# Optimization experiments

Measured on AMD Instinct MI355X. Metric: run time of the kernel, lower is better.

## Reference

```python
import jax, jax.numpy as jnp
import numpy as np


def fwht(x):
    """Normalized fast Walsh-Hadamard transform over the last dim (power of 2).
    Equivalent to x @ H_n / sqrt(n) with H symmetric, so it serves as both
    matmul_hadU and matmul_hadUt in QuIP#."""
    n = x.shape[-1]
    steps = int(np.log2(n))
    assert 1 << steps == n
    shape = x.shape
    x = x.reshape(-1, n)
    h = 1
    for _ in range(steps):
        x = x.reshape(-1, n // (2 * h), 2, h)
        a = x[:, :, 0, :]
        b = x[:, :, 1, :]
        x = jnp.stack([a + b, a - b], axis=2).reshape(-1, n)
        h *= 2
    return (x * np.float32(1.0 / np.sqrt(n))).reshape(shape)


def setup_inputs() -> dict:
    key = jax.random.key(0)
    ks = jax.random.split(key, 9)
    B, S = 4, 2048
    n_in, n_out, codesz, cb_size, rank = 4096, 4096, 4, 256, 64
    inputs = {
        "input": jax.random.normal(ks[0], (B, S, n_in), dtype=jnp.float32),
        "Qidxs": jax.random.randint(ks[1], (n_out, n_in // codesz), 0, cb_size, dtype=jnp.int32),
        "D4_CB": jax.random.normal(ks[2], (cb_size, codesz), dtype=jnp.float32),
        # SU / SV are random sign (+-1) vectors from the randomized Hadamard transform
        "SU": jnp.where(jax.random.bernoulli(ks[3], 0.5, (n_in,)), 1.0, -1.0).astype(jnp.float32),
        "SV": jnp.where(jax.random.bernoulli(ks[4], 0.5, (n_out,)), 1.0, -1.0).astype(jnp.float32),
        "Wscale": jnp.float32(0.9),
        "A": jax.random.normal(ks[5], (n_out, rank), dtype=jnp.float32) * 0.02,
        "B": jax.random.normal(ks[6], (rank, n_in), dtype=jnp.float32) * 0.02,
        # positive per-input-channel rescale
        "scaleWH": jax.random.uniform(ks[7], (n_in,), dtype=jnp.float32, minval=0.5, maxval=1.5),
    }
    return inputs


def reference(input, Qidxs, D4_CB, SU, SV, Wscale, A, B, scaleWH):
    n_out, n_groups = Qidxs.shape
    codesz = D4_CB.shape[1]
    n_in = n_groups * codesz
    lead = input.shape[:-1]

    x = input.reshape(-1, n_in)            # [T, n_in]
    x = x / scaleWH                        # rescale_WH
    x = x * SU                             # input sign flips
    x = fwht(x)                            # matmul_hadUt
    Bx = x @ B.T                           # [T, rank] low-rank path

    # Dequantize: gather codebook vectors and flatten groups -> [n_out, n_in]
    W_hat = D4_CB[Qidxs].reshape(n_out, n_in)
    z = x @ W_hat.T                        # [T, n_out]

    z = z * Wscale
    z = z + Bx @ A.T                       # low-rank correction
    z = fwht(z)                            # matmul_hadU on output dim
    z = z * SV                             # output sign flips
    return z.reshape(*lead, n_out)
```

## Files before the change

kernel.cpp:

```cpp
#include <hip/hip_runtime.h>
#include <hip/hip_bf16.h>
#include <stdint.h>

typedef __attribute__((ext_vector_type(8))) short short8;
typedef __attribute__((ext_vector_type(4))) float floatx4;

#define GLOAD_LDS16(gptr, lptr)                                                     \
  __builtin_amdgcn_global_load_lds(                                                 \
      (const __attribute__((address_space(1))) void*)(gptr),                        \
      (__attribute__((address_space(3))) void*)(lptr), 16, 0, 0)

__device__ inline void fwht16(float v[16]) {
#pragma unroll
    for (int s = 0; s < 4; ++s) {
        const int h = 1 << s;
#pragma unroll
        for (int k = 0; k < 16; k += 2 * h)
#pragma unroll
            for (int j = 0; j < h; ++j) {
                float a = v[k + j], b = v[k + j + h];
                v[k + j] = a + b;
                v[k + j + h] = a - b;
            }
    }
}

__global__ __launch_bounds__(256) void decode_weff(
    const int* __restrict__ Qidxs, const float* __restrict__ D4_CB,
    const float* __restrict__ Wscale_p, const float* __restrict__ A,
    const float* __restrict__ B, __hip_bfloat16* __restrict__ W_eff)
{
    __shared__ __align__(16) float As[64 * 64];
    __shared__ __align__(16) float CB[256 * 4];
    const int t = threadIdx.x;
    const int oBase = blockIdx.y * 64;
    const int iBase = blockIdx.x * 256;

    const float4* A4 = (const float4*)(A + (long)oBase * 64);
    float4* As4 = (float4*)As;
#pragma unroll
    for (int u = 0; u < 4; ++u) As4[t + u * 256] = A4[t + u * 256];
    ((float4*)CB)[t] = ((const float4*)D4_CB)[t];
    __syncthreads();

    const float wscale = Wscale_p[0];
    const int i = iBase + t;
    float bcol[64];
#pragma unroll
    for (int r = 0; r < 64; ++r) bcol[r] = B[r * 4096 + i];

    const int g = i >> 2;
    const int sub = i & 3;

    for (int oo = 0; oo < 64; ++oo) {
        const int o = oBase + oo;
        const float4* arow = (const float4*)&As[oo * 64];
        float acc = 0.f;
#pragma unroll
        for (int r4 = 0; r4 < 16; ++r4) {
            float4 a4 = arow[r4];
            acc += a4.x * bcol[4 * r4 + 0] + a4.y * bcol[4 * r4 + 1] +
                   a4.z * bcol[4 * r4 + 2] + a4.w * bcol[4 * r4 + 3];
        }
        const int q = Qidxs[(long)o * 1024 + g];
        const float w = wscale * CB[q * 4 + sub] + acc;
        W_eff[(long)o * 4096 + i] = __float2bfloat16(w);
    }
}

__global__ __launch_bounds__(256) void fwht_in_kernel(
    const float* __restrict__ x, const float* __restrict__ SU,
    const float* __restrict__ sWH, __hip_bfloat16* __restrict__ xh)
{
    __shared__ float row[4096 + 256];
    const int t = threadIdx.x;
    const long base = (long)blockIdx.x * 4096;
    float v[16];

#pragma unroll
    for (int u = 0; u < 16; ++u) {
        int e = u * 256 + t;
        v[u] = x[base + e] / sWH[e] * SU[e];
    }
    fwht16(v);
#pragma unroll
    for (int u = 0; u < 16; ++u) {
        int e = u * 256 + t;
        row[e + (e >> 4)] = v[u];
    }
    __syncthreads();

    const int lo = t & 15, hi = t >> 4;
#pragma unroll
    for (int u = 0; u < 16; ++u) v[u] = row[hi * 272 + u * 17 + lo];
    fwht16(v);
#pragma unroll
    for (int u = 0; u < 16; ++u) row[hi * 272 + u * 17 + lo] = v[u];
    __syncthreads();

#pragma unroll
    for (int u = 0; u < 16; ++u) v[u] = row[t * 17 + u];
    fwht16(v);

    short8 o0, o1;
#pragma unroll
    for (int u = 0; u < 8; ++u) {
        __hip_bfloat16 b = __float2bfloat16(v[u] * 0.015625f);
        o0[u] = *(short*)&b;
    }
#pragma unroll
    for (int u = 0; u < 8; ++u) {
        __hip_bfloat16 b = __float2bfloat16(v[8 + u] * 0.015625f);
        o1[u] = *(short*)&b;
    }
    *(short8*)(xh + base + t * 16) = o0;
    *(short8*)(xh + base + t * 16 + 8) = o1;
}

__global__ __launch_bounds__(256) void gemm_bt(
    const __hip_bfloat16* __restrict__ xh,
    const __hip_bfloat16* __restrict__ wf,
    __hip_bfloat16* __restrict__ z)
{
    __shared__ __align__(16) __hip_bfloat16 lA[128 * 32];
    __shared__ __align__(16) __hip_bfloat16 lB[128 * 32];
    const int t = threadIdx.x;
    const int lane = t & 63;
    const int wv = t >> 6;
    const int wm = (wv >> 1) * 64;
    const int wn = (wv & 1) * 64;
    const long mBase = (long)blockIdx.y * 128;
    const long nBase = (long)blockIdx.x * 128;

    const int srow = wv * 32 + (lane >> 2);
    const int skoff = (((lane & 3) ^ ((lane >> 3) & 3)) * 8);
    const __hip_bfloat16* gA = xh + (mBase + srow) * 4096 + skoff;
    const __hip_bfloat16* gB = wf + (nBase + srow) * 4096 + skoff;
    const long rstep = 16L * 4096;
    __hip_bfloat16* lA0 = &lA[(wv * 32) * 32];
    __hip_bfloat16* lA1 = &lA[(wv * 32 + 16) * 32];
    __hip_bfloat16* lB0 = &lB[(wv * 32) * 32];
    __hip_bfloat16* lB1 = &lB[(wv * 32 + 16) * 32];

    floatx4 acc[4][4] = {};
    const int fr = lane & 15;
    const int q = lane >> 4;
    const int fq = (q ^ ((fr >> 1) & 3)) * 8;

    for (int kt = 0; kt < 4096; kt += 32) {
        GLOAD_LDS16(gA + kt, lA0);
        GLOAD_LDS16(gA + kt + rstep, lA1);
        GLOAD_LDS16(gB + kt, lB0);
        GLOAD_LDS16(gB + kt + rstep, lB1);
        __syncthreads();

        short8 af[4], bfr[4];
#pragma unroll
        for (int i = 0; i < 4; ++i)
            af[i] = *(const short8*)&lA[(wm + i * 16 + fr) * 32 + fq];
#pragma unroll
        for (int j = 0; j < 4; ++j)
            bfr[j] = *(const short8*)&lB[(wn + j * 16 + fr) * 32 + fq];
#pragma unroll
        for (int i = 0; i < 4; ++i)
#pragma unroll
            for (int j = 0; j < 4; ++j)
                acc[i][j] = __builtin_amdgcn_mfma_f32_16x16x32_bf16(
                    af[i], bfr[j], acc[i][j], 0, 0, 0);
        __syncthreads();
    }

    const int q4 = (lane >> 4) * 4;
#pragma unroll
    for (int i = 0; i < 4; ++i)
#pragma unroll
        for (int j = 0; j < 4; ++j)
#pragma unroll
            for (int r = 0; r < 4; ++r) {
                const long rrow = mBase + wm + i * 16 + q4 + r;
                const long ccol = nBase + wn + j * 16 + fr;
                z[rrow * 4096 + ccol] = __float2bfloat16(acc[i][j][r]);
            }
}

__global__ __launch_bounds__(256) void fwht_out_kernel(
    const __hip_bfloat16* __restrict__ z, const float* __restrict__ SV,
    float* __restrict__ out)
{
    __shared__ float row[4096 + 256];
    const int t = threadIdx.x;
    const long base = (long)blockIdx.x * 4096;
    float v[16];

#pragma unroll
    for (int u = 0; u < 16; ++u) {
        int e = u * 256 + t;
        v[u] = __bfloat162float(z[base + e]);
    }
    fwht16(v);
#pragma unroll
    for (int u = 0; u < 16; ++u) {
        int e = u * 256 + t;
        row[e + (e >> 4)] = v[u];
    }
    __syncthreads();

    const int lo = t & 15, hi = t >> 4;
#pragma unroll
    for (int u = 0; u < 16; ++u) v[u] = row[hi * 272 + u * 17 + lo];
    fwht16(v);
#pragma unroll
    for (int u = 0; u < 16; ++u) row[hi * 272 + u * 17 + lo] = v[u];
    __syncthreads();

#pragma unroll
    for (int u = 0; u < 16; ++u) v[u] = row[t * 17 + u];
    fwht16(v);

    const float4* svv = (const float4*)(SV + t * 16);
    float4* ov = (float4*)(out + base + t * 16);
#pragma unroll
    for (int c = 0; c < 4; ++c) {
        float4 s = svv[c];
        float4 f;
        f.x = v[4 * c + 0] * s.x * 0.015625f;
        f.y = v[4 * c + 1] * s.y * 0.015625f;
        f.z = v[4 * c + 2] * s.z * 0.015625f;
        f.w = v[4 * c + 3] * s.w * 0.015625f;
        ov[c] = f;
    }
}

extern "C" void kernel_launch(void* const* d_in, const int* in_sizes, int n_in,
                              void* d_out, int out_size, void* d_ws, size_t ws_size,
                              hipStream_t stream)
{
    const float* input  = (const float*)d_in[0];
    const int*   Qidxs  = (const int*)d_in[1];
    const float* D4_CB  = (const float*)d_in[2];
    const float* SU     = (const float*)d_in[3];
    const float* SV     = (const float*)d_in[4];
    const float* Wscale = (const float*)d_in[5];
    const float* A      = (const float*)d_in[6];
    const float* B      = (const float*)d_in[7];
    const float* sWH    = (const float*)d_in[8];
    float* out = (float*)d_out;

    char* ws = (char*)d_ws;
    __hip_bfloat16* weff = (__hip_bfloat16*)ws;
    __hip_bfloat16* xh   = (__hip_bfloat16*)(ws + (32L << 20));
    __hip_bfloat16* zbuf = (__hip_bfloat16*)(ws + (32L << 20) + (64L << 20));

    decode_weff<<<dim3(16, 64), 256, 0, stream>>>(Qidxs, D4_CB, Wscale, A, B, weff);
    fwht_in_kernel<<<8192, 256, 0, stream>>>(input, SU, sWH, xh);
    gemm_bt<<<dim3(32, 64), 256, 0, stream>>>(xh, weff, zbuf);
    fwht_out_kernel<<<8192, 256, 0, stream>>>(zbuf, SV, out);
}
```

Measured before the change: 663.1 us.

## Rewrite GEMM as 256x256 double-buffered pipelined tile with 8 waves

Replaces the 128x128, BK=32 single-buffered bf16 GEMM with a 256x256, BK=64 tile run by 512 threads. LDS is double-buffered, and global-to-LDS loads for the next k-step are interleaved with four MFMA quarter-phases using explicit barriers, waitcnt and setprio. The goal is to hide load latency and raise data reuse per LDS byte. It uses 128KB of LDS and many accumulator registers, which limits occupancy, and the hand-managed waitcnt and barriers carry correctness risk.

```diff
diff --git a/kernel.cpp b/kernel.cpp
--- a/kernel.cpp
+++ b/kernel.cpp
@@ -9,6 +9,11 @@
   __builtin_amdgcn_global_load_lds(                                                 \
       (const __attribute__((address_space(1))) void*)(gptr),                        \
       (__attribute__((address_space(3))) void*)(lptr), 16, 0, 0)
+
+#define FENCE() asm volatile("" ::: "memory")
+#define BARRIER() do { FENCE(); __builtin_amdgcn_s_barrier(); FENCE(); } while (0)
+#define WAIT_LGKM0() do { asm volatile("s_waitcnt lgkmcnt(0)" ::: "memory"); \
+                          __builtin_amdgcn_sched_barrier(0); } while (0)
 
 __device__ inline void fwht16(float v[16]) {
 #pragma unroll
@@ -117,69 +122,137 @@
     *(short8*)(xh + base + t * 16 + 8) = o1;
 }
 
-__global__ __launch_bounds__(256) void gemm_bt(
+__global__ __launch_bounds__(512, 2) void gemm_bt(
     const __hip_bfloat16* __restrict__ xh,
     const __hip_bfloat16* __restrict__ wf,
     __hip_bfloat16* __restrict__ z)
 {
-    __shared__ __align__(16) __hip_bfloat16 lA[128 * 32];
-    __shared__ __align__(16) __hip_bfloat16 lB[128 * 32];
+    __shared__ __align__(16) __hip_bfloat16 sA[2][256 * 64];
+    __shared__ __align__(16) __hip_bfloat16 sB[2][256 * 64];
+
     const int t = threadIdx.x;
     const int lane = t & 63;
     const int wv = t >> 6;
-    const int wm = (wv >> 1) * 64;
-    const int wn = (wv & 1) * 64;
-    const long mBase = (long)blockIdx.y * 128;
-    const long nBase = (long)blockIdx.x * 128;
-
-    const int srow = wv * 32 + (lane >> 2);
-    const int skoff = (((lane & 3) ^ ((lane >> 3) & 3)) * 8);
-    const __hip_bfloat16* gA = xh + (mBase + srow) * 4096 + skoff;
-    const __hip_bfloat16* gB = wf + (nBase + srow) * 4096 + skoff;
-    const long rstep = 16L * 4096;
-    __hip_bfloat16* lA0 = &lA[(wv * 32) * 32];
-    __hip_bfloat16* lA1 = &lA[(wv * 32 + 16) * 32];
-    __hip_bfloat16* lB0 = &lB[(wv * 32) * 32];
-    __hip_bfloat16* lB1 = &lB[(wv * 32 + 16) * 32];
-
-    floatx4 acc[4][4] = {};
+    const int wm = wv >> 2;
+    const int wn = wv & 3;
+    const long mBase = (long)blockIdx.y * 256;
+    const long nBase = (long)blockIdx.x * 256;
+
+    const int grow = t >> 3;
+    const int gcol = ((t & 7) ^ (grow & 7)) * 8;
+    const __hip_bfloat16* gA = xh + (mBase + grow) * 4096 + gcol;
+    const __hip_bfloat16* gB = wf + (nBase + grow) * 4096 + gcol;
+    const int lrow = wv * 8;
+
     const int fr = lane & 15;
-    const int q = lane >> 4;
-    const int fq = (q ^ ((fr >> 1) & 3)) * 8;
-
-    for (int kt = 0; kt < 4096; kt += 32) {
-        GLOAD_LDS16(gA + kt, lA0);
-        GLOAD_LDS16(gA + kt + rstep, lA1);
-        GLOAD_LDS16(gB + kt, lB0);
-        GLOAD_LDS16(gB + kt + rstep, lB1);
-        __syncthreads();
-
-        short8 af[4], bfr[4];
-#pragma unroll
-        for (int i = 0; i < 4; ++i)
-            af[i] = *(const short8*)&lA[(wm + i * 16 + fr) * 32 + fq];
-#pragma unroll
-        for (int j = 0; j < 4; ++j)
-            bfr[j] = *(const short8*)&lB[(wn + j * 16 + fr) * 32 + fq];
-#pragma unroll
-        for (int i = 0; i < 4; ++i)
-#pragma unroll
-            for (int j = 0; j < 4; ++j)
-                acc[i][j] = __builtin_amdgcn_mfma_f32_16x16x32_bf16(
-                    af[i], bfr[j], acc[i][j], 0, 0, 0);
-        __syncthreads();
-    }
-
-    const int q4 = (lane >> 4) * 4;
-#pragma unroll
-    for (int i = 0; i < 4; ++i)
-#pragma unroll
-        for (int j = 0; j < 4; ++j)
+    const int c2 = lane >> 4;
+    const int slot0 = ((c2 ^ (fr & 7)) * 8);
+
+    floatx4 acc[8][4] = {};
+    short8 afr[4][2];
+    short8 bfr[4][2];
+
+    auto stage = [&](int buf, int isA, int halfRow, int kt) {
+        const __hip_bfloat16* g =
+            (isA ? gA : gB) + (long)halfRow * 4096 + (long)kt * 64;
+        __hip_bfloat16* l =
+            (isA ? &sA[buf][0] : &sB[buf][0]) + (halfRow + lrow) * 64;
+        GLOAD_LDS16(g, l);
+        GLOAD_LDS16(g + 64L * 4096, l + 64 * 64);
+    };
+    auto ldA = [&](int buf, int mhalf) {
+        const __hip_bfloat16* base =
+            &sA[buf][0] + (wm * 128 + mhalf * 64 + fr) * 64;
+#pragma unroll
+        for (int m = 0; m < 4; ++m) {
+            afr[m][0] = *(const short8*)(base + m * 16 * 64 + slot0);
+            afr[m][1] = *(const short8*)(base + m * 16 * 64 + (slot0 ^ 32));
+        }
+    };
+    auto ldB2 = [&](int buf, int npair) {
+        const __hip_bfloat16* base =
+            &sB[buf][0] + (wn * 64 + npair * 32 + fr) * 64;
+#pragma unroll
+        for (int n = 0; n < 2; ++n) {
+            bfr[npair * 2 + n][0] = *(const short8*)(base + n * 16 * 64 + slot0);
+            bfr[npair * 2 + n][1] = *(const short8*)(base + n * 16 * 64 + (slot0 ^ 32));
+        }
+    };
+    auto mma16 = [&](int mh, int np) {
+#pragma unroll
+        for (int m = 0; m < 4; ++m)
+#pragma unroll
+            for (int n = 0; n < 2; ++n)
+#pragma unroll
+                for (int kh = 0; kh < 2; ++kh)
+                    acc[mh * 4 + m][np * 2 + n] =
+                        __builtin_amdgcn_mfma_f32_16x16x32_bf16(
+                            afr[m][kh], bfr[np * 2 + n][kh],
+                            acc[mh * 4 + m][np * 2 + n], 0, 0, 0);
+    };
+
+    stage(0, 1, 0,   0);
+    stage(0, 1, 128, 0);
+    stage(0, 0, 0,   0);
+    stage(0, 0, 128, 0);
+    stage(1, 0, 0,   1);
+    stage(1, 1, 0,   1);
+    asm volatile("s_waitcnt vmcnt(4)" ::: "memory");
+    BARRIER();
+
+    for (int kt = 0; kt < 64; ++kt) {
+        const int cur = kt & 1;
+
+        ldA(cur, 0);
+        ldB2(cur, 0);
+        if (kt + 1 < 64) stage(cur ^ 1, 1, 128, kt + 1);
+        asm volatile("s_waitcnt lgkmcnt(8)" ::: "memory");
+        BARRIER();
+        WAIT_LGKM0();
+        __builtin_amdgcn_s_setprio(1);
+        mma16(0, 0);
+        __builtin_amdgcn_s_setprio(0);
+        BARRIER();
+
+        ldB2(cur, 1);
+        if (kt + 1 < 64) stage(cur ^ 1, 0, 128, kt + 1);
+        BARRIER();
+        WAIT_LGKM0();
+        __builtin_amdgcn_s_setprio(1);
+        mma16(0, 1);
+        __builtin_amdgcn_s_setprio(0);
+        BARRIER();
+
+        ldA(cur, 1);
+        if (kt + 2 < 64) stage(cur, 0, 0, kt + 2);
+        BARRIER();
+        WAIT_LGKM0();
+        __builtin_amdgcn_s_setprio(1);
+        mma16(1, 0);
+        __builtin_amdgcn_s_setprio(0);
+        BARRIER();
+
+        if (kt + 2 < 64) stage(cur, 1, 0, kt + 2);
+        BARRIER();
+        WAIT_LGKM0();
+        __builtin_amdgcn_s_setprio(1);
+        mma16(1, 1);
+        __builtin_amdgcn_s_setprio(0);
+        if (kt < 62) asm volatile("s_waitcnt vmcnt(4)" ::: "memory");
+        else         asm volatile("s_waitcnt vmcnt(0)" ::: "memory");
+        BARRIER();
+    }
+
+    const int q4 = c2 * 4;
+#pragma unroll
+    for (int m = 0; m < 8; ++m)
+#pragma unroll
+        for (int n = 0; n < 4; ++n)
 #pragma unroll
             for (int r = 0; r < 4; ++r) {
-                const long rrow = mBase + wm + i * 16 + q4 + r;
-                const long ccol = nBase + wn + j * 16 + fr;
-                z[rrow * 4096 + ccol] = __float2bfloat16(acc[i][j][r]);
+                const long row = mBase + wm * 128 + m * 16 + q4 + r;
+                const long col = nBase + wn * 64 + n * 16 + fr;
+                z[row * 4096 + col] = __float2bfloat16(acc[m][n][r]);
             }
 }
 
@@ -253,6 +326,6 @@
 
     decode_weff<<<dim3(16, 64), 256, 0, stream>>>(Qidxs, D4_CB, Wscale, A, B, weff);
     fwht_in_kernel<<<8192, 256, 0, stream>>>(input, SU, sWH, xh);
-    gemm_bt<<<dim3(32, 64), 256, 0, stream>>>(xh, weff, zbuf);
+    gemm_bt<<<dim3(16, 32), 512, 0, stream>>>(xh, weff, zbuf);
     fwht_out_kernel<<<8192, 256, 0, stream>>>(zbuf, SV, out);
 }
```

Result: faster. 613.2 us (-7.5%).
